# Optimization experiments

Hardware: AMD Instinct MI355X
Metric: run time of the kernel (lower is better)

## Reference

```python
import jax, jax.numpy as jnp
import numpy as np

B, Q, PAST = 2, 1024, 1024
T = Q + PAST
HID, NH, NKV, HD = 4096, 32, 8, 128
MAXPOS = 4096
SCALE = HD ** -0.5


def setup_inputs() -> dict:
    key = jax.random.key(0)
    ks = jax.random.split(key, 8)
    hidden_states = jax.random.normal(ks[0], (B, Q, HID), jnp.float32)
    attention_mask = jnp.ones((B, T), jnp.int32)  # all tokens valid
    position_ids = jnp.broadcast_to(
        jnp.arange(PAST, PAST + Q, dtype=jnp.int64)[None, :], (B, Q))
    # standard RoPE caches: [max_pos, head_dim/2]
    inv = 1.0 / (10000.0 ** (np.arange(0, HD, 2, dtype=np.float64) / HD))
    ang = np.arange(MAXPOS, dtype=np.float64)[:, None] * inv[None, :]
    rope_cos_freqs = jnp.asarray(np.cos(ang), jnp.float32)
    rope_sin_freqs = jnp.asarray(np.sin(ang), jnp.float32)
    past_key = jax.random.normal(ks[1], (B, NKV, PAST, HD), jnp.float32)
    past_value = jax.random.normal(ks[2], (B, NKV, PAST, HD), jnp.float32)
    q_w = jax.random.normal(ks[3], (NH * HD, HID), jnp.float32) * 0.02
    k_w = jax.random.normal(ks[4], (NKV * HD, HID), jnp.float32) * 0.02
    v_w = jax.random.normal(ks[5], (NKV * HD, HID), jnp.float32) * 0.02
    o_w = jax.random.normal(ks[6], (HID, NH * HD), jnp.float32) * 0.02
    return {"hidden_states": hidden_states, "attention_mask": attention_mask,
            "position_ids": position_ids, "rope_cos_freqs": rope_cos_freqs,
            "rope_sin_freqs": rope_sin_freqs, "past_key": past_key,
            "past_value": past_value, "q_w": q_w, "k_w": k_w, "v_w": v_w,
            "o_w": o_w}


def _rope(x, cos, sin):
    # x: [B,S,n_heads,HD]; cos/sin: [B,S,HD/2]; non-interleaved (half split)
    d2 = x.shape[-1] // 2
    x1, x2 = x[..., :d2], x[..., d2:]
    c, s = cos[:, :, None, :], sin[:, :, None, :]
    return jnp.concatenate([x1 * c - x2 * s, x2 * c + x1 * s], axis=-1)


def reference(hidden_states, attention_mask, position_ids, rope_cos_freqs,
              rope_sin_freqs, past_key, past_value, q_w, k_w, v_w, o_w):
    b, q_len, _ = hidden_states.shape
    q = jnp.einsum('bsh,oh->bso', hidden_states, q_w).reshape(b, q_len, NH, HD)
    k = jnp.einsum('bsh,oh->bso', hidden_states, k_w).reshape(b, q_len, NKV, HD)
    v = jnp.einsum('bsh,oh->bso', hidden_states, v_w).reshape(b, q_len, NKV, HD)

    cos = rope_cos_freqs[position_ids]  # [B,Q,HD/2]
    sin = rope_sin_freqs[position_ids]
    q = _rope(q, cos, sin)
    k = _rope(k, cos, sin)

    # append to KV cache -> [B,NKV,T,HD]
    present_key = jnp.concatenate([past_key, k.transpose(0, 2, 1, 3)], axis=2)
    present_value = jnp.concatenate([past_value, v.transpose(0, 2, 1, 3)], axis=2)

    # additive causal + padding mask built from cumsum of attention_mask
    all_idx = jnp.cumsum(attention_mask, axis=-1)            # [B,T]
    full = (all_idx[:, -q_len:, None] >= all_idx[:, None, :]) \
        & attention_mask[:, None, :].astype(bool)            # [B,Q,T]
    bias = jnp.where(full, 0.0, -10000.0)[:, None, :, :]     # [B,1,Q,T]

    group = NH // NKV
    k_rep = jnp.repeat(present_key, group, axis=1)           # [B,NH,T,HD]
    v_rep = jnp.repeat(present_value, group, axis=1)

    scores = jnp.einsum('bqhd,bhkd->bhqk', q, k_rep) * SCALE + bias
    probs = jax.nn.softmax(scores, axis=-1)
    ctx = jnp.einsum('bhqk,bhkd->bqhd', probs, v_rep).reshape(b, q_len, NH * HD)
    attn_out = jnp.einsum('bso,ho->bsh', ctx, o_w)
    return attn_out, present_key, present_value
```

## Files before the change

### kernel.cpp

```cpp
#include <hip/hip_runtime.h>
#include <hip/hip_bf16.h>
#include <stdint.h>

typedef __bf16 bf16_t;
typedef bf16_t bf16x8 __attribute__((ext_vector_type(8)));
typedef bf16_t bf16x4 __attribute__((ext_vector_type(4)));
typedef float f32x4 __attribute__((ext_vector_type(4)));

#define B_ 2
#define Q_ 1024
#define PAST_ 1024
#define T_ 2048
#define HID_ 4096
#define NH_ 32
#define NKV_ 8
#define HD_ 128
#define SCALE_ 0.08838834764831845f

__device__ __forceinline__ void async_cp16(const bf16_t* g, bf16_t* l) {
  __builtin_amdgcn_global_load_lds((__attribute__((address_space(1))) void*)g,
                                   (__attribute__((address_space(3))) void*)l, 16, 0, 0);
}

__global__ void cvt_f32_bf16(const float* __restrict__ src, bf16_t* __restrict__ dst, size_t n) {
  size_t i = ((size_t)blockIdx.x * blockDim.x + threadIdx.x) * 8;
  if (i >= n) return;
  float4 a = *(const float4*)(src + i);
  float4 b = *(const float4*)(src + i + 4);
  bf16x8 o;
  o[0] = (bf16_t)a.x; o[1] = (bf16_t)a.y; o[2] = (bf16_t)a.z; o[3] = (bf16_t)a.w;
  o[4] = (bf16_t)b.x; o[5] = (bf16_t)b.y; o[6] = (bf16_t)b.z; o[7] = (bf16_t)b.w;
  *(bf16x8*)(dst + i) = o;
}

__global__ void copy_past(const float* __restrict__ pk, const float* __restrict__ pv,
                          float* __restrict__ oK, float* __restrict__ oV,
                          bf16_t* __restrict__ Kall) {
  size_t i = ((size_t)blockIdx.x * 256 + threadIdx.x) * 4;
  if (i >= (size_t)B_ * NKV_ * PAST_ * HD_) return;
  int d = (int)(i & 127);
  size_t r = i >> 7;
  int t = (int)(r & 1023); r >>= 10;
  int g = (int)(r & 7); int b = (int)(r >> 3);
  size_t dst = (((size_t)b * NKV_ + g) * T_ + t) * HD_ + d;
  float4 k4 = *(const float4*)(pk + i);
  float4 v4 = *(const float4*)(pv + i);
  *(float4*)(oK + dst) = k4;
  *(float4*)(oV + dst) = v4;
  bf16x4 kb; kb[0] = (bf16_t)k4.x; kb[1] = (bf16_t)k4.y; kb[2] = (bf16_t)k4.z; kb[3] = (bf16_t)k4.w;
  *(bf16x4*)(Kall + dst) = kb;
}

__global__ void build_vt(const float* __restrict__ past_v, const float* __restrict__ QKV,
                         bf16_t* __restrict__ Vt) {
  __shared__ bf16_t tile[64][136];
  const int tid = threadIdx.x;
  const int t0 = blockIdx.x * 64, g = blockIdx.y, b = blockIdx.z;
#pragma unroll
  for (int k = 0; k < 8; ++k) {
    int idx = k * 256 + tid;
    int t = idx >> 5, dc = (idx & 31) * 4;
    int tt = t0 + t;
    const float* src = (tt < PAST_)
        ? past_v + ((((size_t)b * NKV_ + g) * PAST_ + tt) * HD_ + dc)
        : QKV + (((size_t)b * Q_ + (tt - PAST_)) * 6144 + 5120 + g * HD_ + dc);
    float4 v4 = *(const float4*)src;
    tile[t][dc] = (bf16_t)v4.x; tile[t][dc + 1] = (bf16_t)v4.y;
    tile[t][dc + 2] = (bf16_t)v4.z; tile[t][dc + 3] = (bf16_t)v4.w;
  }
  __syncthreads();
#pragma unroll
  for (int k = 0; k < 4; ++k) {
    int idx = k * 256 + tid;
    int d = idx >> 3, c = idx & 7;
    bf16x8 o;
#pragma unroll
    for (int j = 0; j < 8; ++j) o[j] = tile[c * 8 + j][d];
    *(bf16x8*)(Vt + ((((size_t)b * NKV_ + g) * HD_ + d) * T_) + t0 + c * 8) = o;
  }
}

__device__ __forceinline__ void stage_tile(const bf16_t* __restrict__ G, int ldg,
                                           bf16_t* __restrict__ L, int tid) {
#pragma unroll
  for (int t = 0; t < 4; ++t) {
    int c = t * 512 + tid;
    int row = c >> 3, sc = (c & 7) ^ (row & 7);
    int cb = t * 512 + (tid & 448);
    async_cp16(G + (size_t)row * ldg + sc * 8, L + (size_t)cb * 8);
  }
}

__device__ __forceinline__ void stage_tileA128(const bf16_t* __restrict__ G, int ldg,
                                               bf16_t* __restrict__ L, int tid) {
#pragma unroll
  for (int t = 0; t < 2; ++t) {
    int c = t * 512 + tid;
    int row = c >> 3, sc = (c & 7) ^ (row & 7);
    int cb = t * 512 + (tid & 448);
    async_cp16(G + (size_t)row * ldg + sc * 8, L + (size_t)cb * 8);
  }
}

__global__ __launch_bounds__(512, 2)
void gemm256(const bf16_t* __restrict__ A, const bf16_t* __restrict__ W,
             float* __restrict__ C, int M, int N, int K) {
  __shared__ bf16_t sm[2][2][16384];
  const int tid = threadIdx.x;
  const int lane = tid & 63;
  const int quad = lane >> 4, l15 = lane & 15;
  const int wave = tid >> 6;
  const int wm = wave >> 2, wn = wave & 3;
  const int bm = blockIdx.y * 256, bn = blockIdx.x * 256;
  const int NT = K >> 6;

  const bf16_t* Ag = A + (size_t)bm * K;
  const bf16_t* Wg = W + (size_t)bn * K;

  f32x4 acc[8][4] = {};

  stage_tile(Ag, K, &sm[0][0][0], tid);
  stage_tile(Wg, K, &sm[0][1][0], tid);
  stage_tile(Ag + 64, K, &sm[1][0][0], tid);
  stage_tile(Wg + 64, K, &sm[1][1][0], tid);
  asm volatile("s_waitcnt vmcnt(8)" ::: "memory");
  __builtin_amdgcn_s_barrier();

  const int arow = wm * 128 + l15;
  const int brow = wn * 64 + l15;
  const int pq = l15 & 7;

  for (int t = 0; t < NT; ++t) {
    const bf16_t* lA = &sm[t & 1][0][0];
    const bf16_t* lB = &sm[t & 1][1][0];
    const int k2 = (t + 2) << 6;
    bf16x8 af[4][2], bf01[2][2], bf23[2][2];

#pragma unroll
    for (int m = 0; m < 4; ++m)
#pragma unroll
      for (int kk = 0; kk < 2; ++kk)
        af[m][kk] = *(const bf16x8*)(lA + (arow + m * 16) * 64 + ((((kk << 2) + quad) ^ pq) << 3));
#pragma unroll
    for (int n = 0; n < 2; ++n)
#pragma unroll
      for (int kk = 0; kk < 2; ++kk)
        bf01[n][kk] = *(const bf16x8*)(lB + (brow + n * 16) * 64 + ((((kk << 2) + quad) ^ pq) << 3));
    __builtin_amdgcn_s_barrier();
    asm volatile("s_waitcnt lgkmcnt(0)" ::: "memory");
    __builtin_amdgcn_sched_barrier(0);
    __builtin_amdgcn_s_setprio(1);
#pragma unroll
    for (int m = 0; m < 4; ++m)
#pragma unroll
      for (int n = 0; n < 2; ++n)
#pragma unroll
        for (int kk = 0; kk < 2; ++kk)
          acc[m][n] = __builtin_amdgcn_mfma_f32_16x16x32_bf16(af[m][kk], bf01[n][kk], acc[m][n], 0, 0, 0);
    __builtin_amdgcn_s_setprio(0);
    __builtin_amdgcn_s_barrier();

#pragma unroll
    for (int n = 0; n < 2; ++n)
#pragma unroll
      for (int kk = 0; kk < 2; ++kk)
        bf23[n][kk] = *(const bf16x8*)(lB + (brow + (n + 2) * 16) * 64 + ((((kk << 2) + quad) ^ pq) << 3));
    __builtin_amdgcn_s_barrier();
    asm volatile("s_waitcnt lgkmcnt(0)" ::: "memory");
    __builtin_amdgcn_sched_barrier(0);
    __builtin_amdgcn_s_setprio(1);
#pragma unroll
    for (int m = 0; m < 4; ++m)
#pragma unroll
      for (int n = 0; n < 2; ++n)
#pragma unroll
        for (int kk = 0; kk < 2; ++kk)
          acc[m][n + 2] = __builtin_amdgcn_mfma_f32_16x16x32_bf16(af[m][kk], bf23[n][kk], acc[m][n + 2], 0, 0, 0);
    __builtin_amdgcn_s_setprio(0);
    __builtin_amdgcn_s_barrier();

#pragma unroll
    for (int m = 0; m < 4; ++m)
#pragma unroll
      for (int kk = 0; kk < 2; ++kk)
        af[m][kk] = *(const bf16x8*)(lA + (arow + (m + 4) * 16) * 64 + ((((kk << 2) + quad) ^ pq) << 3));
    if (t + 2 < NT) stage_tile(Wg + k2, K, &sm[t & 1][1][0], tid);
    __builtin_amdgcn_s_barrier();
    asm volatile("s_waitcnt lgkmcnt(0)" ::: "memory");
    __builtin_amdgcn_sched_barrier(0);
    __builtin_amdgcn_s_setprio(1);
#pragma unroll
    for (int m = 0; m < 4; ++m)
#pragma unroll
      for (int n = 0; n < 2; ++n)
#pragma unroll
        for (int kk = 0; kk < 2; ++kk)
          acc[m + 4][n + 2] = __builtin_amdgcn_mfma_f32_16x16x32_bf16(af[m][kk], bf23[n][kk], acc[m + 4][n + 2], 0, 0, 0);
    __builtin_amdgcn_s_setprio(0);
    __builtin_amdgcn_s_barrier();

    if (t + 2 < NT) stage_tile(Ag + k2, K, &sm[t & 1][0][0], tid);
    __builtin_amdgcn_s_barrier();
    __builtin_amdgcn_s_setprio(1);
#pragma unroll
    for (int m = 0; m < 4; ++m)
#pragma unroll
      for (int n = 0; n < 2; ++n)
#pragma unroll
        for (int kk = 0; kk < 2; ++kk)
          acc[m + 4][n] = __builtin_amdgcn_mfma_f32_16x16x32_bf16(af[m][kk], bf01[n][kk], acc[m + 4][n], 0, 0, 0);
    __builtin_amdgcn_s_setprio(0);
    if (t + 2 < NT)
      asm volatile("s_waitcnt vmcnt(8)" ::: "memory");
    else if (t + 2 == NT)
      asm volatile("s_waitcnt vmcnt(0)" ::: "memory");
    __builtin_amdgcn_s_barrier();
  }

#pragma unroll
  for (int m = 0; m < 8; ++m) {
    int row0 = bm + wm * 128 + m * 16 + quad * 4;
#pragma unroll
    for (int n = 0; n < 4; ++n) {
      int col = bn + wn * 64 + n * 16 + l15;
#pragma unroll
      for (int r = 0; r < 4; ++r)
        C[(size_t)(row0 + r) * N + col] = acc[m][n][r];
    }
  }
}

__global__ __launch_bounds__(512, 2)
void gemm128(const bf16_t* __restrict__ A, const bf16_t* __restrict__ W,
             float* __restrict__ C, int M, int N, int K) {
  __shared__ bf16_t smA[2][8192];
  __shared__ bf16_t smB[2][16384];
  const int tid = threadIdx.x;
  const int lane = tid & 63;
  const int quad = lane >> 4, l15 = lane & 15;
  const int wave = tid >> 6;
  const int wm = wave >> 2, wn = wave & 3;
  const int bm = blockIdx.y * 128, bn = blockIdx.x * 256;
  const int NT = K >> 6;

  const bf16_t* Ag = A + (size_t)bm * K;
  const bf16_t* Wg = W + (size_t)bn * K;

  f32x4 acc[4][4] = {};

  stage_tileA128(Ag, K, &smA[0][0], tid);
  stage_tile(Wg, K, &smB[0][0], tid);
  stage_tileA128(Ag + 64, K, &smA[1][0], tid);
  stage_tile(Wg + 64, K, &smB[1][0], tid);
  asm volatile("s_waitcnt vmcnt(6)" ::: "memory");
  __builtin_amdgcn_s_barrier();

  const int arow = wm * 64 + l15;
  const int brow = wn * 64 + l15;
  const int pq = l15 & 7;

  for (int t = 0; t < NT; ++t) {
    const bf16_t* lA = &smA[t & 1][0];
    const bf16_t* lB = &smB[t & 1][0];
    const int k2 = (t + 2) << 6;
    bf16x8 af[2][2], bf01[2][2], bf23[2][2];

#pragma unroll
    for (int m = 0; m < 2; ++m)
#pragma unroll
      for (int kk = 0; kk < 2; ++kk)
        af[m][kk] = *(const bf16x8*)(lA + (arow + m * 16) * 64 + ((((kk << 2) + quad) ^ pq) << 3));
#pragma unroll
    for (int n = 0; n < 2; ++n)
#pragma unroll
      for (int kk = 0; kk < 2; ++kk)
        bf01[n][kk] = *(const bf16x8*)(lB + (brow + n * 16) * 64 + ((((kk << 2) + quad) ^ pq) << 3));
    __builtin_amdgcn_s_barrier();
    asm volatile("s_waitcnt lgkmcnt(0)" ::: "memory");
    __builtin_amdgcn_sched_barrier(0);
    __builtin_amdgcn_s_setprio(1);
#pragma unroll
    for (int m = 0; m < 2; ++m)
#pragma unroll
      for (int n = 0; n < 2; ++n)
#pragma unroll
        for (int kk = 0; kk < 2; ++kk)
          acc[m][n] = __builtin_amdgcn_mfma_f32_16x16x32_bf16(af[m][kk], bf01[n][kk], acc[m][n], 0, 0, 0);
    __builtin_amdgcn_s_setprio(0);
    __builtin_amdgcn_s_barrier();

#pragma unroll
    for (int n = 0; n < 2; ++n)
#pragma unroll
      for (int kk = 0; kk < 2; ++kk)
        bf23[n][kk] = *(const bf16x8*)(lB + (brow + (n + 2) * 16) * 64 + ((((kk << 2) + quad) ^ pq) << 3));
    __builtin_amdgcn_s_barrier();
    asm volatile("s_waitcnt lgkmcnt(0)" ::: "memory");
    __builtin_amdgcn_sched_barrier(0);
    __builtin_amdgcn_s_setprio(1);
#pragma unroll
    for (int m = 0; m < 2; ++m)
#pragma unroll
      for (int n = 0; n < 2; ++n)
#pragma unroll
        for (int kk = 0; kk < 2; ++kk)
          acc[m][n + 2] = __builtin_amdgcn_mfma_f32_16x16x32_bf16(af[m][kk], bf23[n][kk], acc[m][n + 2], 0, 0, 0);
    __builtin_amdgcn_s_setprio(0);
    __builtin_amdgcn_s_barrier();

#pragma unroll
    for (int m = 0; m < 2; ++m)
#pragma unroll
      for (int kk = 0; kk < 2; ++kk)
        af[m][kk] = *(const bf16x8*)(lA + (arow + (m + 2) * 16) * 64 + ((((kk << 2) + quad) ^ pq) << 3));
    if (t + 2 < NT) stage_tile(Wg + k2, K, &smB[t & 1][0], tid);
    __builtin_amdgcn_s_barrier();
    asm volatile("s_waitcnt lgkmcnt(0)" ::: "memory");
    __builtin_amdgcn_sched_barrier(0);
    __builtin_amdgcn_s_setprio(1);
#pragma unroll
    for (int m = 0; m < 2; ++m)
#pragma unroll
      for (int n = 0; n < 2; ++n)
#pragma unroll
        for (int kk = 0; kk < 2; ++kk)
          acc[m + 2][n + 2] = __builtin_amdgcn_mfma_f32_16x16x32_bf16(af[m][kk], bf23[n][kk], acc[m + 2][n + 2], 0, 0, 0);
    __builtin_amdgcn_s_setprio(0);
    __builtin_amdgcn_s_barrier();

    if (t + 2 < NT) stage_tileA128(Ag + k2, K, &smA[t & 1][0], tid);
    __builtin_amdgcn_s_barrier();
    __builtin_amdgcn_s_setprio(1);
#pragma unroll
    for (int m = 0; m < 2; ++m)
#pragma unroll
      for (int n = 0; n < 2; ++n)
#pragma unroll
        for (int kk = 0; kk < 2; ++kk)
          acc[m + 2][n] = __builtin_amdgcn_mfma_f32_16x16x32_bf16(af[m][kk], bf01[n][kk], acc[m + 2][n], 0, 0, 0);
    __builtin_amdgcn_s_setprio(0);
    if (t + 2 < NT)
      asm volatile("s_waitcnt vmcnt(6)" ::: "memory");
    else if (t + 2 == NT)
      asm volatile("s_waitcnt vmcnt(0)" ::: "memory");
    __builtin_amdgcn_s_barrier();
  }

#pragma unroll
  for (int m = 0; m < 4; ++m) {
    int row0 = bm + wm * 64 + m * 16 + quad * 4;
#pragma unroll
    for (int n = 0; n < 4; ++n) {
      int col = bn + wn * 64 + n * 16 + l15;
#pragma unroll
      for (int r = 0; r < 4; ++r)
        C[(size_t)(row0 + r) * N + col] = acc[m][n][r];
    }
  }
}

__global__ void rope_scatter(const float* __restrict__ QKV, const float* __restrict__ cosf,
                             const float* __restrict__ sinf, const int* __restrict__ pos_ids,
                             bf16_t* __restrict__ Qr, bf16_t* __restrict__ Kall,
                             float* __restrict__ outK, float* __restrict__ outV) {
  int m = blockIdx.x;
  int b = m >> 10, s = m & 1023;
  int pos = pos_ids[(size_t)b * Q_ + s];
  const float* row = QKV + (size_t)m * 6144;
  int tid = threadIdx.x;
  for (int p = tid; p < NH_ * 64; p += 256) {
    int h = p >> 6, d = p & 63;
    float x1 = row[h * 128 + d], x2 = row[h * 128 + d + 64];
    float c = cosf[pos * 64 + d], sn = sinf[pos * 64 + d];
    size_t qb = (((size_t)b * NH_ + h) * Q_ + s) * HD_;
    Qr[qb + d] = (bf16_t)((x1 * c - x2 * sn) * SCALE_);
    Qr[qb + d + 64] = (bf16_t)((x2 * c + x1 * sn) * SCALE_);
  }
  for (int p = tid; p < NKV_ * 64; p += 256) {
    int g = p >> 6, d = p & 63;
    float x1 = row[4096 + g * 128 + d], x2 = row[4096 + g * 128 + d + 64];
    float c = cosf[pos * 64 + d], sn = sinf[pos * 64 + d];
    float o1 = x1 * c - x2 * sn, o2 = x2 * c + x1 * sn;
    size_t kbi = (((size_t)b * NKV_ + g) * T_ + PAST_ + s) * HD_;
    Kall[kbi + d] = (bf16_t)o1; Kall[kbi + d + 64] = (bf16_t)o2;
    outK[kbi + d] = o1; outK[kbi + d + 64] = o2;
  }
  for (int e = tid; e < NKV_ * HD_; e += 256) {
    int g = e >> 7, d = e & 127;
    float v = row[5120 + g * 128 + d];
    outV[(((size_t)b * NKV_ + g) * T_ + PAST_ + s) * HD_ + d] = v;
  }
}

__global__ __launch_bounds__(512, 2)
void attn_fwd(const bf16_t* __restrict__ Qr, const bf16_t* __restrict__ Kall,
              const bf16_t* __restrict__ Vt, bf16_t* __restrict__ Ctx) {
  __shared__ bf16_t lK[2][64 * 128];
  __shared__ bf16_t lV[2][128 * 64];
  __shared__ bf16_t lP[8 * 16 * 64];
  const int tid = threadIdx.x;
  const int wave = tid >> 6, lane = tid & 63;
  const int quad = lane >> 4, l15 = lane & 15;
  const int i = blockIdx.x;
  const int xcd = i & 7;
  const int j = i >> 3;
  const int pairsel = j & 1;
  const int idx = j >> 1;
  const int h_in = idx & 3;
  const int qt = 7 - (idx >> 2);
  const int b = pairsel, kv = xcd;
  const int h = kv * 4 + h_in;
  const int qbase = qt * 128;
  const int wq = qbase + wave * 16;
  const size_t kvbase = ((size_t)b * NKV_ + kv) * T_ * HD_;
  const size_t vtbase = ((size_t)b * NKV_ + kv) * HD_ * T_;

  auto stageKV = [&](int kb, int s) {
#pragma unroll
    for (int t = 0; t < 2; ++t) {
      int c = t * 512 + tid;
      int row = c >> 4, sc = (c & 15) ^ (row & 15);
      int cb = t * 512 + (tid & 448);
      async_cp16(Kall + kvbase + (size_t)(kb + row) * HD_ + sc * 8, lK[s] + (size_t)cb * 8);
    }
#pragma unroll
    for (int t = 0; t < 2; ++t) {
      int c = t * 512 + tid;
      int d = c >> 3, sc = (c & 7) ^ (d & 7);
      int cb = t * 512 + (tid & 448);
      async_cp16(Vt + vtbase + (size_t)d * T_ + kb + sc * 8, lV[s] + (size_t)cb * 8);
    }
  };

  bf16x8 qf[4];
  {
    const bf16_t* qg = Qr + ((((size_t)b * NH_ + h) * Q_) + wq + l15) * HD_ + quad * 8;
#pragma unroll
    for (int kk = 0; kk < 4; ++kk) qf[kk] = *(const bf16x8*)(qg + kk * 32);
  }
  f32x4 ctx[8] = {};
  float Mr[4], Lr[4];
#pragma unroll
  for (int r = 0; r < 4; ++r) { Mr[r] = -3.0e30f; Lr[r] = 0.0f; }
  bf16_t* lPw = lP + wave * 16 * 64;
  const int nt = (PAST_ + qbase + 128) >> 6;
  const int wlimit = PAST_ + wq + 15;

  stageKV(0, 0);

  for (int ti = 0; ti < nt; ++ti) {
    const int kb = ti << 6;
    const int cur = ti & 1;
    if (ti + 1 < nt) {
      stageKV(kb + 64, cur ^ 1);
      asm volatile("s_waitcnt vmcnt(4)" ::: "memory");
    } else {
      asm volatile("s_waitcnt vmcnt(0)" ::: "memory");
    }
    __builtin_amdgcn_s_barrier();
    asm volatile("" ::: "memory");
    if (kb <= wlimit) {
      const bf16_t* cK = lK[cur];
      const bf16_t* cV = lV[cur];
      f32x4 sacc[4];
#pragma unroll
      for (int nc = 0; nc < 4; ++nc) sacc[nc] = (f32x4){0.f, 0.f, 0.f, 0.f};
      __builtin_amdgcn_s_setprio(1);
#pragma unroll
      for (int nc = 0; nc < 4; ++nc)
#pragma unroll
        for (int kk = 0; kk < 4; ++kk) {
          bf16x8 bk = *(const bf16x8*)(cK + (nc * 16 + l15) * 128 + (((kk * 4 + quad) ^ l15) << 3));
          sacc[nc] = __builtin_amdgcn_mfma_f32_16x16x32_bf16(qf[kk], bk, sacc[nc], 0, 0, 0);
        }
      __builtin_amdgcn_s_setprio(0);
      bool fullvis = (kb + 63 <= PAST_ + wq);
      if (!fullvis) {
#pragma unroll
        for (int nc = 0; nc < 4; ++nc) {
          int tkey = kb + nc * 16 + l15;
#pragma unroll
          for (int r = 0; r < 4; ++r)
            if (tkey > PAST_ + wq + quad * 4 + r) sacc[nc][r] -= 10000.0f;
        }
      }
      float tmax[4];
      bool need = false;
#pragma unroll
      for (int r = 0; r < 4; ++r) {
        float tm = fmaxf(fmaxf(sacc[0][r], sacc[1][r]), fmaxf(sacc[2][r], sacc[3][r]));
#pragma unroll
        for (int mmk = 1; mmk < 16; mmk <<= 1) tm = fmaxf(tm, __shfl_xor(tm, mmk, 64));
        tmax[r] = tm;
        need = need || (tm > Mr[r] + 8.0f);
      }
      if (__any(need)) {
#pragma unroll
        for (int r = 0; r < 4; ++r) {
          float nm = fmaxf(Mr[r], tmax[r]);
          float al = __expf(Mr[r] - nm);
          Mr[r] = nm;
          Lr[r] *= al;
#pragma unroll
          for (int nc2 = 0; nc2 < 8; ++nc2) ctx[nc2][r] *= al;
        }
      }
      float rs[4] = {};
#pragma unroll
      for (int nc = 0; nc < 4; ++nc)
#pragma unroll
        for (int r = 0; r < 4; ++r) {
          float p = __expf(sacc[nc][r] - Mr[r]);
          rs[r] += p;
          int rho = quad * 4 + r;
          int cslot = ((nc * 2 + (l15 >> 3)) ^ (rho & 7));
          lPw[rho * 64 + cslot * 8 + (l15 & 7)] = (bf16_t)p;
        }
#pragma unroll
      for (int r = 0; r < 4; ++r) {
        float s = rs[r];
#pragma unroll
        for (int mmk = 1; mmk < 16; mmk <<= 1) s += __shfl_xor(s, mmk, 64);
        Lr[r] += s;
      }
      asm volatile("s_waitcnt lgkmcnt(0)" ::: "memory");
      __builtin_amdgcn_sched_barrier(0);
      __builtin_amdgcn_s_setprio(1);
#pragma unroll
      for (int kk2 = 0; kk2 < 2; ++kk2) {
        bf16x8 ap = *(const bf16x8*)(lPw + l15 * 64 + (((kk2 * 4 + quad) ^ (l15 & 7)) << 3));
#pragma unroll
        for (int nc2 = 0; nc2 < 8; ++nc2) {
          bf16x8 bv = *(const bf16x8*)(cV + (nc2 * 16 + l15) * 64 + (((kk2 * 4 + quad) ^ (l15 & 7)) << 3));
          ctx[nc2] = __builtin_amdgcn_mfma_f32_16x16x32_bf16(ap, bv, ctx[nc2], 0, 0, 0);
        }
      }
      __builtin_amdgcn_s_setprio(0);
    }
    __builtin_amdgcn_sched_barrier(0);
    __builtin_amdgcn_s_barrier();
  }
  float inv[4];
#pragma unroll
  for (int r = 0; r < 4; ++r) inv[r] = 1.0f / Lr[r];
#pragma unroll
  for (int nc2 = 0; nc2 < 8; ++nc2)
#pragma unroll
    for (int r = 0; r < 4; ++r) {
      size_t row = (size_t)b * Q_ + wq + quad * 4 + r;
      Ctx[row * (NH_ * HD_) + h * HD_ + nc2 * 16 + l15] = (bf16_t)(ctx[nc2][r] * inv[r]);
    }
}

extern "C" void kernel_launch(void* const* d_in, const int* in_sizes, int n_in,
                              void* d_out, int out_size, void* d_ws, size_t ws_size,
                              hipStream_t stream) {
  const float* hidden = (const float*)d_in[0];
  const int* pos = (const int*)d_in[2];
  const float* cosf = (const float*)d_in[3];
  const float* sinf = (const float*)d_in[4];
  const float* past_k = (const float*)d_in[5];
  const float* past_v = (const float*)d_in[6];
  const float* q_w = (const float*)d_in[7];
  const float* k_w = (const float*)d_in[8];
  const float* v_w = (const float*)d_in[9];
  const float* o_w = (const float*)d_in[10];

  float* attn_out = (float*)d_out;
  float* outK = attn_out + (size_t)B_ * Q_ * HID_;
  float* outV = outK + (size_t)B_ * NKV_ * T_ * HD_;

  if (ws_size < 150994944) return;
  char* ws = (char*)d_ws;
  bf16_t* Wqkv = (bf16_t*)(ws);
  bf16_t* Xb   = (bf16_t*)(ws + 50331648);
  float*  QKV  = (float*)(ws + 67108864);
  bf16_t* Qr   = (bf16_t*)(ws + 117440512);
  bf16_t* Kall = (bf16_t*)(ws + 134217728);
  bf16_t* Vt   = (bf16_t*)(ws + 142606336);
  bf16_t* Wo   = (bf16_t*)(ws + 67108864);
  bf16_t* Ctx  = (bf16_t*)(ws + 50331648);

  cvt_f32_bf16<<<4096, 256, 0, stream>>>(hidden, Xb, 8388608);
  cvt_f32_bf16<<<8192, 256, 0, stream>>>(q_w, Wqkv, 16777216);
  cvt_f32_bf16<<<2048, 256, 0, stream>>>(k_w, Wqkv + 16777216, 4194304);
  cvt_f32_bf16<<<2048, 256, 0, stream>>>(v_w, Wqkv + 20971520, 4194304);
  copy_past<<<2048, 256, 0, stream>>>(past_k, past_v, outK, outV, Kall);
  gemm256<<<dim3(24, 8), 512, 0, stream>>>(Xb, Wqkv, QKV, 2048, 6144, 4096);
  rope_scatter<<<2048, 256, 0, stream>>>(QKV, cosf, sinf, pos, Qr, Kall, outK, outV);
  build_vt<<<dim3(32, 8, 2), 256, 0, stream>>>(past_v, QKV, Vt);
  cvt_f32_bf16<<<8192, 256, 0, stream>>>(o_w, Wo, 16777216);
  attn_fwd<<<512, 512, 0, stream>>>(Qr, Kall, Vt, Ctx);
  gemm128<<<dim3(16, 16), 512, 0, stream>>>(Ctx, Wo, attn_out, 2048, 4096, 4096);
}
```

Measured before the change: 580.7 us.

## Process two 16-row query groups per wave and compute row sums via MFMA

Each wave now handles 32 query rows (two groups of 16) instead of 16, so every K and V fragment read from LDS feeds two MFMAs, and each block covers 256 query rows, halving the grid to 256 blocks. The softmax row sums now come from MFMA against a ones vector rather than cross-lane shuffle reductions. This halves K/V global and LDS traffic per query but doubles register pressure (two context accumulators) and leaves fewer blocks, which risks spills, lower occupancy and worse load balance across the causal triangle on a 256-CU device.

New measurement: 568.2 us. 1.02x faster.

```diff
diff --git a/kernel.cpp b/kernel.cpp
--- a/kernel.cpp
+++ b/kernel.cpp
@@ -397,7 +397,7 @@
               const bf16_t* __restrict__ Vt, bf16_t* __restrict__ Ctx) {
   __shared__ bf16_t lK[2][64 * 128];
   __shared__ bf16_t lV[2][128 * 64];
-  __shared__ bf16_t lP[8 * 16 * 64];
+  __shared__ bf16_t lP[8 * 2 * 16 * 64];
   const int tid = threadIdx.x;
   const int wave = tid >> 6, lane = tid & 63;
   const int quad = lane >> 4, l15 = lane & 15;
@@ -407,11 +407,11 @@
   const int pairsel = j & 1;
   const int idx = j >> 1;
   const int h_in = idx & 3;
-  const int qt = 7 - (idx >> 2);
+  const int qt = 3 - (idx >> 2);
   const int b = pairsel, kv = xcd;
   const int h = kv * 4 + h_in;
-  const int qbase = qt * 128;
-  const int wq = qbase + wave * 16;
+  const int qbase = qt * 256;
+  const int wq = qbase + wave * 32;
   const size_t kvbase = ((size_t)b * NKV_ + kv) * T_ * HD_;
   const size_t vtbase = ((size_t)b * NKV_ + kv) * HD_ * T_;
 
@@ -432,19 +432,26 @@
     }
   };
 
-  bf16x8 qf[4];
-  {
-    const bf16_t* qg = Qr + ((((size_t)b * NH_ + h) * Q_) + wq + l15) * HD_ + quad * 8;
-#pragma unroll
-    for (int kk = 0; kk < 4; ++kk) qf[kk] = *(const bf16x8*)(qg + kk * 32);
-  }
-  f32x4 ctx[8] = {};
-  float Mr[4], Lr[4];
-#pragma unroll
-  for (int r = 0; r < 4; ++r) { Mr[r] = -3.0e30f; Lr[r] = 0.0f; }
-  bf16_t* lPw = lP + wave * 16 * 64;
-  const int nt = (PAST_ + qbase + 128) >> 6;
-  const int wlimit = PAST_ + wq + 15;
+  bf16x8 qf[2][4];
+#pragma unroll
+  for (int g = 0; g < 2; ++g) {
+    const bf16_t* qg = Qr + ((((size_t)b * NH_ + h) * Q_) + wq + g * 16 + l15) * HD_ + quad * 8;
+#pragma unroll
+    for (int kk = 0; kk < 4; ++kk) qf[g][kk] = *(const bf16x8*)(qg + kk * 32);
+  }
+  bf16x8 ones;
+#pragma unroll
+  for (int e = 0; e < 8; ++e) ones[e] = (bf16_t)1.0f;
+
+  f32x4 ctx[2][8] = {};
+  float Mr[2][4], Lr[2][4];
+#pragma unroll
+  for (int g = 0; g < 2; ++g)
+#pragma unroll
+    for (int r = 0; r < 4; ++r) { Mr[g][r] = -3.0e30f; Lr[g][r] = 0.0f; }
+  bf16_t* lPw0 = lP + wave * 2048;
+  bf16_t* lPw1 = lPw0 + 1024;
+  const int nt = (PAST_ + qbase + 256) >> 6;
 
   stageKV(0, 0);
 
@@ -459,97 +466,123 @@
     }
     __builtin_amdgcn_s_barrier();
     asm volatile("" ::: "memory");
-    if (kb <= wlimit) {
+    if (kb <= PAST_ + wq + 31) {
       const bf16_t* cK = lK[cur];
       const bf16_t* cV = lV[cur];
-      f32x4 sacc[4];
-#pragma unroll
-      for (int nc = 0; nc < 4; ++nc) sacc[nc] = (f32x4){0.f, 0.f, 0.f, 0.f};
+      f32x4 sacc[2][4];
+#pragma unroll
+      for (int g = 0; g < 2; ++g)
+#pragma unroll
+        for (int nc = 0; nc < 4; ++nc) sacc[g][nc] = (f32x4){0.f, 0.f, 0.f, 0.f};
       __builtin_amdgcn_s_setprio(1);
 #pragma unroll
-      for (int nc = 0; nc < 4; ++nc)
-#pragma unroll
-        for (int kk = 0; kk < 4; ++kk) {
-          bf16x8 bk = *(const bf16x8*)(cK + (nc * 16 + l15) * 128 + (((kk * 4 + quad) ^ l15) << 3));
-          sacc[nc] = __builtin_amdgcn_mfma_f32_16x16x32_bf16(qf[kk], bk, sacc[nc], 0, 0, 0);
+      for (int nc = 0; nc < 4; ++nc) {
+        bf16x8 bk[4];
+#pragma unroll
+        for (int kk = 0; kk < 4; ++kk)
+          bk[kk] = *(const bf16x8*)(cK + (nc * 16 + l15) * 128 + (((kk * 4 + quad) ^ l15) << 3));
+#pragma unroll
+        for (int kk = 0; kk < 4; ++kk)
+          sacc[0][nc] = __builtin_amdgcn_mfma_f32_16x16x32_bf16(qf[0][kk], bk[kk], sacc[0][nc], 0, 0, 0);
+#pragma unroll
+        for (int kk = 0; kk < 4; ++kk)
+          sacc[1][nc] = __builtin_amdgcn_mfma_f32_16x16x32_bf16(qf[1][kk], bk[kk], sacc[1][nc], 0, 0, 0);
+      }
+      __builtin_amdgcn_s_setprio(0);
+      bool need = false;
+      float tmax[2][4];
+#pragma unroll
+      for (int g = 0; g < 2; ++g) {
+        int wqg = wq + g * 16;
+        bool fullvis = (kb + 63 <= PAST_ + wqg);
+        if (!fullvis) {
+#pragma unroll
+          for (int nc = 0; nc < 4; ++nc) {
+            int tkey = kb + nc * 16 + l15;
+#pragma unroll
+            for (int r = 0; r < 4; ++r)
+              if (tkey > PAST_ + wqg + quad * 4 + r) sacc[g][nc][r] -= 10000.0f;
+          }
         }
-      __builtin_amdgcn_s_setprio(0);
-      bool fullvis = (kb + 63 <= PAST_ + wq);
-      if (!fullvis) {
-#pragma unroll
-        for (int nc = 0; nc < 4; ++nc) {
-          int tkey = kb + nc * 16 + l15;
-#pragma unroll
-          for (int r = 0; r < 4; ++r)
-            if (tkey > PAST_ + wq + quad * 4 + r) sacc[nc][r] -= 10000.0f;
+#pragma unroll
+        for (int r = 0; r < 4; ++r) {
+          float tm = fmaxf(fmaxf(sacc[g][0][r], sacc[g][1][r]), fmaxf(sacc[g][2][r], sacc[g][3][r]));
+#pragma unroll
+          for (int mmk = 1; mmk < 16; mmk <<= 1) tm = fmaxf(tm, __shfl_xor(tm, mmk, 64));
+          tmax[g][r] = tm;
+          need = need || (tm > Mr[g][r] + 8.0f);
         }
       }
-      float tmax[4];
-      bool need = false;
-#pragma unroll
-      for (int r = 0; r < 4; ++r) {
-        float tm = fmaxf(fmaxf(sacc[0][r], sacc[1][r]), fmaxf(sacc[2][r], sacc[3][r]));
-#pragma unroll
-        for (int mmk = 1; mmk < 16; mmk <<= 1) tm = fmaxf(tm, __shfl_xor(tm, mmk, 64));
-        tmax[r] = tm;
-        need = need || (tm > Mr[r] + 8.0f);
+      if (__any(need)) {
+#pragma unroll
+        for (int g = 0; g < 2; ++g)
+#pragma unroll
+          for (int r = 0; r < 4; ++r) {
+            float nm = fmaxf(Mr[g][r], tmax[g][r]);
+            float al = __expf(Mr[g][r] - nm);
+            Mr[g][r] = nm;
+            Lr[g][r] *= al;
+#pragma unroll
+            for (int nc2 = 0; nc2 < 8; ++nc2) ctx[g][nc2][r] *= al;
+          }
       }
-      if (__any(need)) {
-#pragma unroll
-        for (int r = 0; r < 4; ++r) {
-          float nm = fmaxf(Mr[r], tmax[r]);
-          float al = __expf(Mr[r] - nm);
-          Mr[r] = nm;
-          Lr[r] *= al;
-#pragma unroll
-          for (int nc2 = 0; nc2 < 8; ++nc2) ctx[nc2][r] *= al;
-        }
-      }
-      float rs[4] = {};
-#pragma unroll
-      for (int nc = 0; nc < 4; ++nc)
-#pragma unroll
-        for (int r = 0; r < 4; ++r) {
-          float p = __expf(sacc[nc][r] - Mr[r]);
-          rs[r] += p;
-          int rho = quad * 4 + r;
-          int cslot = ((nc * 2 + (l15 >> 3)) ^ (rho & 7));
-          lPw[rho * 64 + cslot * 8 + (l15 & 7)] = (bf16_t)p;
-        }
-#pragma unroll
-      for (int r = 0; r < 4; ++r) {
-        float s = rs[r];
-#pragma unroll
-        for (int mmk = 1; mmk < 16; mmk <<= 1) s += __shfl_xor(s, mmk, 64);
-        Lr[r] += s;
+#pragma unroll
+      for (int g = 0; g < 2; ++g) {
+        bf16_t* lPw = g ? lPw1 : lPw0;
+#pragma unroll
+        for (int nc = 0; nc < 4; ++nc)
+#pragma unroll
+          for (int r = 0; r < 4; ++r) {
+            float p = __expf(sacc[g][nc][r] - Mr[g][r]);
+            int rho = quad * 4 + r;
+            int cslot = ((nc * 2 + (l15 >> 3)) ^ (rho & 7));
+            lPw[rho * 64 + cslot * 8 + (l15 & 7)] = (bf16_t)p;
+          }
       }
       asm volatile("s_waitcnt lgkmcnt(0)" ::: "memory");
       __builtin_amdgcn_sched_barrier(0);
+      bf16x8 ap0[2], ap1[2];
+#pragma unroll
+      for (int kk2 = 0; kk2 < 2; ++kk2) {
+        int off = (((kk2 * 4 + quad) ^ (l15 & 7)) << 3);
+        ap0[kk2] = *(const bf16x8*)(lPw0 + l15 * 64 + off);
+        ap1[kk2] = *(const bf16x8*)(lPw1 + l15 * 64 + off);
+      }
       __builtin_amdgcn_s_setprio(1);
+      f32x4 ls0 = (f32x4){0.f, 0.f, 0.f, 0.f}, ls1 = (f32x4){0.f, 0.f, 0.f, 0.f};
 #pragma unroll
       for (int kk2 = 0; kk2 < 2; ++kk2) {
-        bf16x8 ap = *(const bf16x8*)(lPw + l15 * 64 + (((kk2 * 4 + quad) ^ (l15 & 7)) << 3));
-#pragma unroll
-        for (int nc2 = 0; nc2 < 8; ++nc2) {
+        ls0 = __builtin_amdgcn_mfma_f32_16x16x32_bf16(ap0[kk2], ones, ls0, 0, 0, 0);
+        ls1 = __builtin_amdgcn_mfma_f32_16x16x32_bf16(ap1[kk2], ones, ls1, 0, 0, 0);
+      }
+#pragma unroll
+      for (int nc2 = 0; nc2 < 8; ++nc2)
+#pragma unroll
+        for (int kk2 = 0; kk2 < 2; ++kk2) {
           bf16x8 bv = *(const bf16x8*)(cV + (nc2 * 16 + l15) * 64 + (((kk2 * 4 + quad) ^ (l15 & 7)) << 3));
-          ctx[nc2] = __builtin_amdgcn_mfma_f32_16x16x32_bf16(ap, bv, ctx[nc2], 0, 0, 0);
+          ctx[0][nc2] = __builtin_amdgcn_mfma_f32_16x16x32_bf16(ap0[kk2], bv, ctx[0][nc2], 0, 0, 0);
+          ctx[1][nc2] = __builtin_amdgcn_mfma_f32_16x16x32_bf16(ap1[kk2], bv, ctx[1][nc2], 0, 0, 0);
         }
-      }
       __builtin_amdgcn_s_setprio(0);
+#pragma unroll
+      for (int r = 0; r < 4; ++r) { Lr[0][r] += ls0[r]; Lr[1][r] += ls1[r]; }
     }
     __builtin_amdgcn_sched_barrier(0);
     __builtin_amdgcn_s_barrier();
   }
-  float inv[4];
-#pragma unroll
-  for (int r = 0; r < 4; ++r) inv[r] = 1.0f / Lr[r];
-#pragma unroll
-  for (int nc2 = 0; nc2 < 8; ++nc2)
-#pragma unroll
-    for (int r = 0; r < 4; ++r) {
-      size_t row = (size_t)b * Q_ + wq + quad * 4 + r;
-      Ctx[row * (NH_ * HD_) + h * HD_ + nc2 * 16 + l15] = (bf16_t)(ctx[nc2][r] * inv[r]);
-    }
+#pragma unroll
+  for (int g = 0; g < 2; ++g) {
+    float inv[4];
+#pragma unroll
+    for (int r = 0; r < 4; ++r) inv[r] = 1.0f / Lr[g][r];
+#pragma unroll
+    for (int nc2 = 0; nc2 < 8; ++nc2)
+#pragma unroll
+      for (int r = 0; r < 4; ++r) {
+        size_t row = (size_t)b * Q_ + wq + g * 16 + quad * 4 + r;
+        Ctx[row * (NH_ * HD_) + h * HD_ + nc2 * 16 + l15] = (bf16_t)(ctx[g][nc2][r] * inv[r]);
+      }
+  }
 }
 
 extern "C" void kernel_launch(void* const* d_in, const int* in_sizes, int n_in,
@@ -590,6 +623,6 @@
   rope_scatter<<<2048, 256, 0, stream>>>(QKV, cosf, sinf, pos, Qr, Kall, outK, outV);
   build_vt<<<dim3(32, 8, 2), 256, 0, stream>>>(past_v, QKV, Vt);
   cvt_f32_bf16<<<8192, 256, 0, stream>>>(o_w, Wo, 16777216);
-  attn_fwd<<<512, 512, 0, stream>>>(Qr, Kall, Vt, Ctx);
+  attn_fwd<<<256, 512, 0, stream>>>(Qr, Kall, Vt, Ctx);
   gemm128<<<dim3(16, 16), 512, 0, stream>>>(Ctx, Wo, attn_out, 2048, 4096, 4096);
 }
```
